# Optimization experiments

Hardware: AMD Instinct MI355X
Metric: run time of the kernel (lower is better)

The kernel has to match this reference:

```python
import jax, jax.numpy as jnp
import numpy as np

B, N, C, H = 8, 4096, 768, 8


def setup_inputs() -> dict:
    key = jax.random.key(0)
    k1, k2, k3 = jax.random.split(key, 3)
    x = jax.random.normal(k1, (B, N, C), dtype=jnp.float32)
    W_qkv = jax.random.normal(k2, (C, 3 * C), dtype=jnp.float32) * 0.02
    W_proj = jax.random.normal(k3, (C, C), dtype=jnp.float32) * 0.02
    b_proj = jnp.zeros((C,), dtype=jnp.float32)
    temp = jnp.ones((H, 1, 1), dtype=jnp.float32)
    return {"x": x, "W_qkv": W_qkv, "W_proj": W_proj, "b_proj": b_proj, "temp": temp}


def reference(x, W_qkv, W_proj, b_proj, temp):
    b, n, c = x.shape
    h = temp.shape[0]
    d = c // h
    # qkv: [B,N,3C] -> [B,N,H,D,3]  (matches tf.reshape split order)
    qkv = (x @ W_qkv).reshape(b, n, h, d, 3)
    q, k, v = qkv[..., 0], qkv[..., 1], qkv[..., 2]
    # L2-normalize along the patch axis (axis=1), as tf.linalg.normalize
    q = q / jnp.linalg.norm(q, axis=1, keepdims=True)
    k = k / jnp.linalg.norm(k, axis=1, keepdims=True)
    # channel-wise (cross-covariance) attention: [B,H,D,D]
    attn = jnp.einsum('bnhd,bnhe->bhde', q, k) * temp
    attn = jax.nn.softmax(attn, axis=-1)
    # apply to v and fold heads back: [B,N,C]
    y = jnp.einsum('bhde,bnhe->bnhd', attn, v).reshape(b, n, c)
    return y @ W_proj + b_proj
```

## Files before the change

### kernel.cpp

```cpp
#include <hip/hip_runtime.h>

typedef __attribute__((ext_vector_type(8))) short short8;
typedef __attribute__((ext_vector_type(4))) float f32x4;

__device__ inline unsigned short f2b(float f) {
  unsigned int u = __builtin_bit_cast(unsigned int, f);
  u = (u + 0x7FFFu + ((u >> 16) & 1u)) >> 16;
  return (unsigned short)u;
}
__device__ inline float b2f(unsigned short s) {
  unsigned int u = ((unsigned int)s) << 16;
  return __builtin_bit_cast(float, u);
}

__device__ inline void async16(const void* g, void* l) {
  __builtin_amdgcn_global_load_lds((__attribute__((address_space(1))) void*)(g),
                                   (__attribute__((address_space(3))) void*)(l), 16, 0, 0);
}

__global__ void cvt_x(const float4* __restrict__ x, ushort4* __restrict__ xb, int n4) {
  int i = blockIdx.x * blockDim.x + threadIdx.x;
  int stride = gridDim.x * blockDim.x;
  for (; i < n4; i += stride) {
    float4 v = x[i];
    ushort4 o;
    o.x = f2b(v.x); o.y = f2b(v.y); o.z = f2b(v.z); o.w = f2b(v.w);
    xb[i] = o;
  }
}

__global__ __launch_bounds__(256) void t_wqkv(const float* __restrict__ W, unsigned short* __restrict__ Wt) {
  __shared__ float tile[32][33];
  int j0 = blockIdx.x * 32, c0 = blockIdx.y * 32;
  int tx = threadIdx.x & 31, ty = threadIdx.x >> 5;
#pragma unroll
  for (int r = 0; r < 32; r += 8)
    tile[ty + r][tx] = W[(size_t)(c0 + ty + r) * 2304 + j0 + tx];
  __syncthreads();
#pragma unroll
  for (int r = 0; r < 32; r += 8) {
    int j = j0 + ty + r;
    int h = j / 288, rem = j - h * 288;
    int d = rem / 3, s = rem - d * 3;
    int jj = s * 768 + h * 96 + d;
    Wt[(size_t)jj * 768 + c0 + tx] = f2b(tile[tx][ty + r]);
  }
}

__global__ __launch_bounds__(256) void t_wproj(const float* __restrict__ W, unsigned short* __restrict__ Wt) {
  __shared__ float tile[32][33];
  int j0 = blockIdx.x * 32, c0 = blockIdx.y * 32;
  int tx = threadIdx.x & 31, ty = threadIdx.x >> 5;
#pragma unroll
  for (int r = 0; r < 32; r += 8)
    tile[ty + r][tx] = W[(size_t)(c0 + ty + r) * 768 + j0 + tx];
  __syncthreads();
#pragma unroll
  for (int r = 0; r < 32; r += 8)
    Wt[(size_t)(j0 + ty + r) * 768 + c0 + tx] = f2b(tile[tx][ty + r]);
}

__global__ __launch_bounds__(256) void gemm_qkv(
    const unsigned short* __restrict__ A, const unsigned short* __restrict__ Bt,
    unsigned short* __restrict__ Q, unsigned short* __restrict__ Kd, unsigned short* __restrict__ V) {
  __shared__ __align__(16) unsigned short As[128 * 64];
  __shared__ __align__(16) unsigned short Bs[128 * 64];
  const int tid = threadIdx.x;
  const int wave = tid >> 6, lane = tid & 63;
  const int mlane = lane & 15, quad = lane >> 4;
  const int m0 = blockIdx.x * 128, n0 = blockIdx.y * 128;
  const int wm = (wave >> 1) * 64, wn = (wave & 1) * 64;
  f32x4 acc[4][4] = {};
  for (int k0 = 0; k0 < 768; k0 += 64) {
    __syncthreads();
#pragma unroll
    for (int t = 0; t < 4; ++t) {
      int ebase = t * 256 + (wave << 6);
      int e = ebase + lane;
      int row = e >> 3, c8 = e & 7;
      async16(A + (size_t)(m0 + row) * 768 + k0 + c8 * 8, As + ebase * 8);
      async16(Bt + (size_t)(n0 + row) * 768 + k0 + c8 * 8, Bs + ebase * 8);
    }
    __syncthreads();
#pragma unroll
    for (int kk = 0; kk < 64; kk += 32) {
      short8 a[4], b[4];
#pragma unroll
      for (int f = 0; f < 4; ++f)
        a[f] = *(const short8*)&As[(wm + f * 16 + mlane) * 64 + kk + quad * 8];
#pragma unroll
      for (int f = 0; f < 4; ++f)
        b[f] = *(const short8*)&Bs[(wn + f * 16 + mlane) * 64 + kk + quad * 8];
#pragma unroll
      for (int i = 0; i < 4; ++i)
#pragma unroll
        for (int j = 0; j < 4; ++j)
          acc[i][j] = __builtin_amdgcn_mfma_f32_16x16x32_bf16(a[i], b[j], acc[i][j], 0, 0, 0);
    }
  }
  const int bb = m0 >> 12;
  const int nb = (m0 & 4095) + wm + quad * 4;
#pragma unroll
  for (int fn = 0; fn < 4; ++fn) {
    int jj = n0 + wn + fn * 16 + mlane;
    int s = jj / 768;
    int hd = jj - s * 768;
    int h = hd / 96;
    int d = hd - h * 96;
    unsigned short* dst = (s == 0) ? Q : (s == 1) ? Kd : V;
    size_t colbase = ((size_t)(bb * 8 + h) * 4096) * 96 + d;
#pragma unroll
    for (int fm = 0; fm < 4; ++fm) {
      int n = nb + fm * 16;
#pragma unroll
      for (int r = 0; r < 4; ++r)
        dst[colbase + (size_t)(n + r) * 96] = f2b(acc[fm][fn][r]);
    }
  }
}

__global__ __launch_bounds__(256) void attn_partial(
    const unsigned short* __restrict__ Q, const unsigned short* __restrict__ Kd,
    float* __restrict__ Spart, float* __restrict__ sq, float* __restrict__ sk) {
  int chunk = blockIdx.x;
  int bh = blockIdx.y;
  __shared__ __align__(16) unsigned short QT[96 * 72];
  __shared__ __align__(16) unsigned short KT[96 * 72];
  int t = threadIdx.x;
  int wave = t >> 6, lane = t & 63, mlane = lane & 15, quad = lane >> 4;
  int wrow = (wave >> 1) * 48, wcol = (wave & 1) * 48;
  f32x4 acc[3][3] = {};
  const unsigned int* qp = (const unsigned int*)(Q + (size_t)bh * 4096 * 96);
  const unsigned int* kp = (const unsigned int*)(Kd + (size_t)bh * 4096 * 96);
  int c = t % 48, rg = t / 48;
  int nbeg = chunk * 256;
  float aq0 = 0.f, aq1 = 0.f, ak0 = 0.f, ak1 = 0.f;
  for (int n0 = nbeg; n0 < nbeg + 256; n0 += 64) {
    __syncthreads();
    if (rg < 5) {
      for (int n = rg; n < 64; n += 5) {
        unsigned int qv = qp[(size_t)(n0 + n) * 48 + c];
        unsigned int kv = kp[(size_t)(n0 + n) * 48 + c];
        QT[(2 * c) * 72 + n] = (unsigned short)(qv & 0xffff);
        QT[(2 * c + 1) * 72 + n] = (unsigned short)(qv >> 16);
        KT[(2 * c) * 72 + n] = (unsigned short)(kv & 0xffff);
        KT[(2 * c + 1) * 72 + n] = (unsigned short)(kv >> 16);
        float q0 = b2f((unsigned short)(qv & 0xffff)), q1 = b2f((unsigned short)(qv >> 16));
        float k0 = b2f((unsigned short)(kv & 0xffff)), k1 = b2f((unsigned short)(kv >> 16));
        aq0 += q0 * q0; aq1 += q1 * q1; ak0 += k0 * k0; ak1 += k1 * k1;
      }
    }
    __syncthreads();
#pragma unroll
    for (int kk = 0; kk < 64; kk += 32) {
      short8 a[3], bf[3];
#pragma unroll
      for (int f = 0; f < 3; ++f)
        a[f] = *(const short8*)&QT[(wrow + f * 16 + mlane) * 72 + kk + quad * 8];
#pragma unroll
      for (int f = 0; f < 3; ++f)
        bf[f] = *(const short8*)&KT[(wcol + f * 16 + mlane) * 72 + kk + quad * 8];
#pragma unroll
      for (int i = 0; i < 3; ++i)
#pragma unroll
        for (int j = 0; j < 3; ++j)
          acc[i][j] = __builtin_amdgcn_mfma_f32_16x16x32_bf16(a[i], bf[j], acc[i][j], 0, 0, 0);
    }
  }
  if (rg < 5) {
    atomicAdd(&sq[bh * 96 + 2 * c], aq0);
    atomicAdd(&sq[bh * 96 + 2 * c + 1], aq1);
    atomicAdd(&sk[bh * 96 + 2 * c], ak0);
    atomicAdd(&sk[bh * 96 + 2 * c + 1], ak1);
  }
  float* dst = Spart + ((size_t)bh * 16 + chunk) * 9216;
#pragma unroll
  for (int i = 0; i < 3; ++i)
#pragma unroll
    for (int j = 0; j < 3; ++j)
#pragma unroll
      for (int r = 0; r < 4; ++r)
        dst[(wrow + i * 16 + quad * 4 + r) * 96 + wcol + j * 16 + mlane] = acc[i][j][r];
}

__global__ __launch_bounds__(256) void attn_finalize(
    const float* __restrict__ Spart, const float* __restrict__ sq,
    const float* __restrict__ sk, const float* __restrict__ temp,
    unsigned short* __restrict__ P) {
  int bh = blockIdx.x, h = bh & 7;
  __shared__ float S[9216];
  __shared__ float rk[96], rq[96];
  int t = threadIdx.x;
  const float* base = Spart + (size_t)bh * 16 * 9216;
  if (t < 96) {
    rk[t] = rsqrtf(sk[bh * 96 + t]);
    rq[t] = rsqrtf(sq[bh * 96 + t]) * temp[h];
  }
  __syncthreads();
  for (int i = t; i < 9216; i += 256) {
    float s = 0.f;
#pragma unroll
    for (int c2 = 0; c2 < 16; ++c2) s += base[(size_t)c2 * 9216 + i];
    int d = i / 96, e = i - d * 96;
    S[i] = s * rq[d] * rk[e];
  }
  __syncthreads();
  if (t < 96) {
    int d = t;
    float mx = -1e30f;
    for (int e = 0; e < 96; ++e) mx = fmaxf(mx, S[d * 96 + e]);
    float sum = 0.f;
    for (int e = 0; e < 96; ++e) {
      float v = expf(S[d * 96 + e] - mx);
      S[d * 96 + e] = v;
      sum += v;
    }
    float inv = 1.0f / sum;
    for (int e = 0; e < 96; ++e)
      P[(size_t)bh * 9216 + d * 96 + e] = f2b(S[d * 96 + e] * inv);
  }
}

__global__ __launch_bounds__(256) void gemm_pv(
    const unsigned short* __restrict__ V, const unsigned short* __restrict__ P,
    unsigned short* __restrict__ y) {
  int bh = blockIdx.y;
  int b = bh >> 3, h = bh & 7;
  int m0 = blockIdx.x * 128;
  int t = threadIdx.x, wave = t >> 6, lane = t & 63, mlane = lane & 15, quad = lane >> 4;
  const unsigned short* Vb = V + (size_t)bh * 4096 * 96;
  const unsigned short* Pb = P + (size_t)bh * 9216;
  f32x4 acc[2][6] = {};
#pragma unroll
  for (int kk = 0; kk < 96; kk += 32) {
    short8 a[2], bfr[6];
#pragma unroll
    for (int i = 0; i < 2; ++i)
      a[i] = *(const short8*)&Vb[(size_t)(m0 + wave * 32 + i * 16 + mlane) * 96 + kk + quad * 8];
#pragma unroll
    for (int j = 0; j < 6; ++j)
      bfr[j] = *(const short8*)&Pb[(j * 16 + mlane) * 96 + kk + quad * 8];
#pragma unroll
    for (int i = 0; i < 2; ++i)
#pragma unroll
      for (int j = 0; j < 6; ++j)
        acc[i][j] = __builtin_amdgcn_mfma_f32_16x16x32_bf16(a[i], bfr[j], acc[i][j], 0, 0, 0);
  }
#pragma unroll
  for (int i = 0; i < 2; ++i) {
    int n = m0 + wave * 32 + i * 16 + quad * 4;
#pragma unroll
    for (int j = 0; j < 6; ++j) {
      int d = j * 16 + mlane;
#pragma unroll
      for (int r = 0; r < 4; ++r)
        y[((size_t)b * 4096 + n + r) * 768 + h * 96 + d] = f2b(acc[i][j][r]);
    }
  }
}

__global__ __launch_bounds__(256) void gemm_proj(
    const unsigned short* __restrict__ A, const unsigned short* __restrict__ Bt,
    const float* __restrict__ bias, float* __restrict__ out) {
  __shared__ __align__(16) unsigned short As[128 * 64];
  __shared__ __align__(16) unsigned short Bs[128 * 64];
  const int tid = threadIdx.x;
  const int wave = tid >> 6, lane = tid & 63;
  const int mlane = lane & 15, quad = lane >> 4;
  const int m0 = blockIdx.x * 128, n0 = blockIdx.y * 128;
  const int wm = (wave >> 1) * 64, wn = (wave & 1) * 64;
  f32x4 acc[4][4] = {};
  for (int k0 = 0; k0 < 768; k0 += 64) {
    __syncthreads();
#pragma unroll
    for (int t = 0; t < 4; ++t) {
      int ebase = t * 256 + (wave << 6);
      int e = ebase + lane;
      int row = e >> 3, c8 = e & 7;
      async16(A + (size_t)(m0 + row) * 768 + k0 + c8 * 8, As + ebase * 8);
      async16(Bt + (size_t)(n0 + row) * 768 + k0 + c8 * 8, Bs + ebase * 8);
    }
    __syncthreads();
#pragma unroll
    for (int kk = 0; kk < 64; kk += 32) {
      short8 a[4], b[4];
#pragma unroll
      for (int f = 0; f < 4; ++f)
        a[f] = *(const short8*)&As[(wm + f * 16 + mlane) * 64 + kk + quad * 8];
#pragma unroll
      for (int f = 0; f < 4; ++f)
        b[f] = *(const short8*)&Bs[(wn + f * 16 + mlane) * 64 + kk + quad * 8];
#pragma unroll
      for (int i = 0; i < 4; ++i)
#pragma unroll
        for (int j = 0; j < 4; ++j)
          acc[i][j] = __builtin_amdgcn_mfma_f32_16x16x32_bf16(a[i], b[j], acc[i][j], 0, 0, 0);
    }
  }
#pragma unroll
  for (int fn = 0; fn < 4; ++fn) {
    int col = n0 + wn + fn * 16 + mlane;
    float bv = bias[col];
#pragma unroll
    for (int fm = 0; fm < 4; ++fm) {
      int m = m0 + wm + fm * 16 + quad * 4;
#pragma unroll
      for (int r = 0; r < 4; ++r)
        out[(size_t)(m + r) * 768 + col] = acc[fm][fn][r] + bv;
    }
  }
}

extern "C" void kernel_launch(void* const* d_in, const int* in_sizes, int n_in,
                              void* d_out, int out_size, void* d_ws, size_t ws_size,
                              hipStream_t stream) {
  const float* x = (const float*)d_in[0];
  const float* Wqkv = (const float*)d_in[1];
  const float* Wproj = (const float*)d_in[2];
  const float* bias = (const float*)d_in[3];
  const float* temp = (const float*)d_in[4];
  float* out = (float*)d_out;

  char* ws = (char*)d_ws;
  size_t off = 0;
  auto alloc = [&](size_t bytes) -> void* {
    void* p = ws + off;
    off += (bytes + 255) & ~(size_t)255;
    return p;
  };
  unsigned short* xb = (unsigned short*)alloc(32768ull * 768 * 2);
  unsigned short* Wtq = (unsigned short*)alloc(2304ull * 768 * 2);
  unsigned short* Wtp = (unsigned short*)alloc(768ull * 768 * 2);
  unsigned short* Q = (unsigned short*)alloc(64ull * 4096 * 96 * 2);
  unsigned short* Kd = (unsigned short*)alloc(64ull * 4096 * 96 * 2);
  unsigned short* V = (unsigned short*)alloc(64ull * 4096 * 96 * 2);
  float* sq = (float*)alloc(64 * 96 * 4);
  float* sk = (float*)alloc(64 * 96 * 4);
  unsigned short* P = (unsigned short*)alloc(64ull * 9216 * 2);
  (void)off; (void)ws_size; (void)in_sizes; (void)n_in; (void)out_size;

  float* Spart = out;

  cvt_x<<<4096, 256, 0, stream>>>((const float4*)x, (ushort4*)xb, 32768 * 768 / 4);
  t_wqkv<<<dim3(72, 24), 256, 0, stream>>>(Wqkv, Wtq);
  t_wproj<<<dim3(24, 24), 256, 0, stream>>>(Wproj, Wtp);
  hipMemsetAsync(sq, 0, 64 * 96 * 4, stream);
  hipMemsetAsync(sk, 0, 64 * 96 * 4, stream);
  gemm_qkv<<<dim3(256, 18), 256, 0, stream>>>(xb, Wtq, Q, Kd, V);
  attn_partial<<<dim3(16, 64), 256, 0, stream>>>(Q, Kd, Spart, sq, sk);
  attn_finalize<<<64, 256, 0, stream>>>(Spart, sq, sk, temp, P);
  gemm_pv<<<dim3(32, 64), 256, 0, stream>>>(V, P, xb );
  gemm_proj<<<dim3(256, 6), 256, 0, stream>>>(xb , Wtp, bias, out);
}
```

Before: 540.1 us.

## Rewrite QKV GEMM with 256x256 tiles and double-buffered async LDS pipeline

The QKV projection GEMM moves from 128x128 tiles with 256 threads to 256x256 tiles with 512 threads. It uses 128 KB of dynamic shared memory as two stages, prefetching the next K-tile with async global-to-LDS loads while MFMAs run on the current one. Explicit waitcnt/barrier placement and setprio are added around the MFMA block. The aim is to raise arithmetic intensity and hide memory latency. The cost is higher register pressure (128 accumulator floats per thread) and fewer blocks in the grid (1152), which lowers occupancy.

```diff
diff --git a/kernel.cpp b/kernel.cpp
--- a/kernel.cpp
+++ b/kernel.cpp
@@ -60,49 +60,93 @@
     Wt[(size_t)(j0 + ty + r) * 768 + c0 + tx] = f2b(tile[tx][ty + r]);
 }
 
-__global__ __launch_bounds__(256) void gemm_qkv(
+__global__ __launch_bounds__(512, 2) void gemm_qkv(
     const unsigned short* __restrict__ A, const unsigned short* __restrict__ Bt,
     unsigned short* __restrict__ Q, unsigned short* __restrict__ Kd, unsigned short* __restrict__ V) {
-  __shared__ __align__(16) unsigned short As[128 * 64];
-  __shared__ __align__(16) unsigned short Bs[128 * 64];
+  extern __shared__ __align__(16) unsigned short smem[];
   const int tid = threadIdx.x;
   const int wave = tid >> 6, lane = tid & 63;
   const int mlane = lane & 15, quad = lane >> 4;
-  const int m0 = blockIdx.x * 128, n0 = blockIdx.y * 128;
-  const int wm = (wave >> 1) * 64, wn = (wave & 1) * 64;
-  f32x4 acc[4][4] = {};
-  for (int k0 = 0; k0 < 768; k0 += 64) {
-    __syncthreads();
-#pragma unroll
-    for (int t = 0; t < 4; ++t) {
-      int ebase = t * 256 + (wave << 6);
+  const int m0 = blockIdx.x * 256, n0 = blockIdx.y * 256;
+  const int wm = (wave >> 2) * 128;
+  const int wn = (wave & 3) * 64;
+
+  f32x4 acc[8][4] = {};
+
+  auto stage = [&](int kt, int c) {
+    const int k0 = kt * 64;
+    unsigned short* As_c = smem + c * 32768;
+    unsigned short* Bs_c = As_c + 16384;
+#pragma unroll
+    for (int i = 0; i < 4; ++i) {
+      int ebase = i * 512 + (wave << 6);
       int e = ebase + lane;
-      int row = e >> 3, c8 = e & 7;
-      async16(A + (size_t)(m0 + row) * 768 + k0 + c8 * 8, As + ebase * 8);
-      async16(Bt + (size_t)(n0 + row) * 768 + k0 + c8 * 8, Bs + ebase * 8);
-    }
-    __syncthreads();
-#pragma unroll
-    for (int kk = 0; kk < 64; kk += 32) {
-      short8 a[4], b[4];
-#pragma unroll
-      for (int f = 0; f < 4; ++f)
-        a[f] = *(const short8*)&As[(wm + f * 16 + mlane) * 64 + kk + quad * 8];
-#pragma unroll
-      for (int f = 0; f < 4; ++f)
-        b[f] = *(const short8*)&Bs[(wn + f * 16 + mlane) * 64 + kk + quad * 8];
-#pragma unroll
-      for (int i = 0; i < 4; ++i)
-#pragma unroll
-        for (int j = 0; j < 4; ++j)
-          acc[i][j] = __builtin_amdgcn_mfma_f32_16x16x32_bf16(a[i], b[j], acc[i][j], 0, 0, 0);
-    }
-  }
+      int row = e >> 3, slot = e & 7;
+      async16(A + (size_t)(m0 + row) * 768 + k0 + slot * 8, As_c + (size_t)ebase * 8);
+      async16(Bt + (size_t)(n0 + row) * 768 + k0 + slot * 8, Bs_c + (size_t)ebase * 8);
+    }
+  };
+
+  stage(0, 0);
+  stage(1, 1);
+  asm volatile("s_waitcnt vmcnt(8)" ::: "memory");
+  __builtin_amdgcn_s_barrier();
+
+#pragma unroll 1
+  for (int t = 0; t < 12; ++t) {
+    const int c = t & 1;
+    const unsigned short* As_c = smem + c * 32768;
+    const unsigned short* Bs_c = As_c + 16384;
+
+    short8 af[2][2][4];
+    short8 bf[2][4];
+#pragma unroll
+    for (int mh = 0; mh < 2; ++mh)
+#pragma unroll
+      for (int kk = 0; kk < 2; ++kk)
+#pragma unroll
+        for (int f = 0; f < 4; ++f)
+          af[mh][kk][f] = *(const short8*)&As_c[(wm + mh * 64 + f * 16 + mlane) * 64 + kk * 32 + quad * 8];
+#pragma unroll
+    for (int kk = 0; kk < 2; ++kk)
+#pragma unroll
+      for (int j = 0; j < 4; ++j)
+        bf[kk][j] = *(const short8*)&Bs_c[(wn + j * 16 + mlane) * 64 + kk * 32 + quad * 8];
+
+    if (t < 10) {
+      asm volatile("s_waitcnt lgkmcnt(0)" ::: "memory");
+      __builtin_amdgcn_sched_barrier(0);
+      __builtin_amdgcn_s_barrier();
+      stage(t + 2, c);
+    }
+
+    __builtin_amdgcn_s_setprio(1);
+#pragma unroll
+    for (int kk = 0; kk < 2; ++kk)
+#pragma unroll
+      for (int mh = 0; mh < 2; ++mh)
+#pragma unroll
+        for (int f = 0; f < 4; ++f)
+#pragma unroll
+          for (int j = 0; j < 4; ++j)
+            acc[mh * 4 + f][j] =
+                __builtin_amdgcn_mfma_f32_16x16x32_bf16(af[mh][kk][f], bf[kk][j], acc[mh * 4 + f][j], 0, 0, 0);
+    __builtin_amdgcn_s_setprio(0);
+
+    if (t < 10) {
+      asm volatile("s_waitcnt vmcnt(8)" ::: "memory");
+      __builtin_amdgcn_s_barrier();
+    } else if (t == 10) {
+      asm volatile("s_waitcnt vmcnt(0)" ::: "memory");
+      __builtin_amdgcn_s_barrier();
+    }
+  }
+
   const int bb = m0 >> 12;
   const int nb = (m0 & 4095) + wm + quad * 4;
 #pragma unroll
-  for (int fn = 0; fn < 4; ++fn) {
-    int jj = n0 + wn + fn * 16 + mlane;
+  for (int j = 0; j < 4; ++j) {
+    int jj = n0 + wn + j * 16 + mlane;
     int s = jj / 768;
     int hd = jj - s * 768;
     int h = hd / 96;
@@ -110,11 +154,11 @@
     unsigned short* dst = (s == 0) ? Q : (s == 1) ? Kd : V;
     size_t colbase = ((size_t)(bb * 8 + h) * 4096) * 96 + d;
 #pragma unroll
-    for (int fm = 0; fm < 4; ++fm) {
-      int n = nb + fm * 16;
+    for (int mf = 0; mf < 8; ++mf) {
+      int n = nb + (mf >> 2) * 64 + (mf & 3) * 16;
 #pragma unroll
       for (int r = 0; r < 4; ++r)
-        dst[colbase + (size_t)(n + r) * 96] = f2b(acc[fm][fn][r]);
+        dst[colbase + (size_t)(n + r) * 96] = f2b(acc[mf][j][r]);
     }
   }
 }
@@ -341,12 +385,18 @@
 
   float* Spart = out;
 
+  static bool attr_set = false;
+  if (!attr_set) {
+    hipFuncSetAttribute((const void*)gemm_qkv, hipFuncAttributeMaxDynamicSharedMemorySize, 131072);
+    attr_set = true;
+  }
+
   cvt_x<<<4096, 256, 0, stream>>>((const float4*)x, (ushort4*)xb, 32768 * 768 / 4);
   t_wqkv<<<dim3(72, 24), 256, 0, stream>>>(Wqkv, Wtq);
   t_wproj<<<dim3(24, 24), 256, 0, stream>>>(Wproj, Wtp);
   hipMemsetAsync(sq, 0, 64 * 96 * 4, stream);
   hipMemsetAsync(sk, 0, 64 * 96 * 4, stream);
-  gemm_qkv<<<dim3(256, 18), 256, 0, stream>>>(xb, Wtq, Q, Kd, V);
+  gemm_qkv<<<dim3(128, 9), 512, 131072, stream>>>(xb, Wtq, Q, Kd, V);
   attn_partial<<<dim3(16, 64), 256, 0, stream>>>(Q, Kd, Spart, sq, sk);
   attn_finalize<<<64, 256, 0, stream>>>(Spart, sq, sk, temp, P);
   gemm_pv<<<dim3(32, 64), 256, 0, stream>>>(V, P, xb );
```

After: 552.3 us. +2.2%, slower.
